# Optimization experiments

Hardware: AMD Instinct MI355X
Metric: run time of the kernel (lower is better)

## Reference

```python
import jax, jax.numpy as jnp
import numpy as np

N = 768          # number of atoms
DIM = 3
F = 128          # feature width
N_RBF = 32       # gaussian radial basis size
CUTOFF = 5.0
NUM_CHAINS = 4
T_IN_K = 300.0
TTIME = 20.0
KB = 8.617330337217213e-05   # Boltzmann constant, eV/K (ASE units.kB)
BOX = 24.8                   # box side so that ~26 neighbors/atom within cutoff
GAMMA = 1.0 / (CUTOFF / N_RBF) ** 2  # RBF width


def setup_inputs() -> dict:
    key = jax.random.key(0)
    ks = jax.random.split(key, 12)
    q = jax.random.uniform(ks[0], (N, DIM), dtype=jnp.float32) * BOX
    v = jax.random.normal(ks[1], (N, DIM), dtype=jnp.float32) * 0.01
    p_eta = jax.random.normal(ks[2], (NUM_CHAINS,), dtype=jnp.float32) * 0.1
    mass = jax.random.uniform(ks[3], (N,), dtype=jnp.float32, minval=1.0, maxval=20.0)
    atomic_numbers = jax.random.randint(ks[4], (N,), 0, 100, dtype=jnp.int32)
    embed = jax.random.normal(ks[5], (100, F), dtype=jnp.float32) * 0.1
    W1 = jax.random.normal(ks[6], (N_RBF, F), dtype=jnp.float32) / np.sqrt(N_RBF)
    b1 = jnp.zeros((F,), dtype=jnp.float32)
    W2 = jax.random.normal(ks[7], (F, F), dtype=jnp.float32) / np.sqrt(F)
    b2 = jnp.zeros((F,), dtype=jnp.float32)
    W3 = jax.random.normal(ks[8], (F, F), dtype=jnp.float32) / np.sqrt(F)
    w_out = jax.random.normal(ks[9], (F,), dtype=jnp.float32) / np.sqrt(F)
    return dict(v=v, q=q, p_eta=p_eta, mass=mass, embed=embed, W1=W1, b1=b1,
                W2=W2, b2=b2, W3=W3, w_out=w_out, atomic_numbers=atomic_numbers)


def _energy(q, atomic_numbers, embed, W1, b1, W2, b2, W3, w_out):
    """SchNet-style cutoff-graph potential energy (scalar)."""
    h = embed[atomic_numbers]                                   # [N,F]
    disp = q[:, None, :] - q[None, :, :]                        # [N,N,3]
    d2 = jnp.sum(disp * disp, axis=-1)                          # [N,N]
    eye = jnp.eye(N, dtype=bool)
    mask = (d2 < CUTOFF ** 2) & (~eye)                          # cutoff neighbor list (dense mask)
    d = jnp.sqrt(jnp.where(mask, d2, 1.0))                      # safe sqrt off-graph
    centers = jnp.linspace(0.0, CUTOFF, N_RBF, dtype=q.dtype)
    rbf = jnp.exp(-GAMMA * (d[..., None] - centers) ** 2)       # [N,N,n_rbf]
    filt = jax.nn.relu(rbf @ W1 + b1) @ W2 + b2                 # [N,N,F]
    filt = jnp.where(mask[..., None], filt, 0.0)
    m = jnp.einsum('ijf,jf->if', filt, h)                       # message aggregation
    h = h + jax.nn.relu(m @ W3)
    return jnp.sum(h @ w_out)


def reference(v, q, p_eta, mass, embed, W1, b1, W2, b2, W3, w_out, atomic_numbers):
    kT = T_IN_K * KB
    n_dof = N * DIM
    target_ke = 0.5 * n_dof * kT
    Q = 2.0 * jnp.array([n_dof * kT * TTIME ** 2] + [kT * TTIME ** 2] * (NUM_CHAINS - 1),
                        dtype=v.dtype)
    p = v * mass[:, None]                                       # momenta
    current_ke = 0.5 * jnp.sum(p * p / mass[:, None])
    # f = -dE/dq (torch: -results['energy_grad'])
    f = -jax.grad(_energy)(q, atomic_numbers, embed, W1, b1, W2, b2, W3, w_out)
    coupled_forces = (p_eta[0] * p.reshape(-1) / Q[0]).reshape(-1, 3)
    dvdt = (f - coupled_forces) / mass[:, None]
    dpeta_first = 2.0 * (current_ke - target_ke) - p_eta[0] * p_eta[1] / Q[1]
    dpeta_mid = p_eta[:-2] ** 2 / Q[:-2] - kT - p_eta[1:-1] * p_eta[2:] / Q[2:]
    dpeta_last = p_eta[-2] ** 2 / Q[-2] - kT
    dpeta_dt = jnp.concatenate([dpeta_first[None], dpeta_mid, dpeta_last[None]])
    return (dvdt, v, dpeta_dt)
```

## Files before the change

kernel.cpp:

```cpp
#include <hip/hip_runtime.h>
#include <math.h>

#define N_ATOMS 768
#define FD 128
#define NRBF 32
#define MAXN 64
#define PPF 32
#define NTHREADS 512
#define TST 136
#define RSTU 40

constexpr float  CUT2   = 25.0f;
constexpr float  GAMMA_ = 40.96f;
constexpr float  CSTEP  = 5.0f / 31.0f;
constexpr double KB_D   = 8.617330337217213e-05;
constexpr double KT_D   = 300.0 * KB_D;
constexpr float  KT_F   = (float)KT_D;
constexpr float  TARGET_KE = (float)(0.5 * 2304.0 * KT_D);
constexpr float  Q0_F   = (float)(2.0 * 2304.0 * KT_D * 400.0);
constexpr float  QI_F   = (float)(2.0 * KT_D * 400.0);

#define DVDT_OFF 0
#define V_OFF    (3 * N_ATOMS)
#define PETA_OFF (6 * N_ATOMS)

using short8v = __attribute__((ext_vector_type(8))) short;
using f32x4   = __attribute__((ext_vector_type(4))) float;

#define MFMA_B16 __builtin_amdgcn_mfma_f32_16x16x32_bf16

__device__ __forceinline__ unsigned short f2bf(float x) {
    unsigned int u = __float_as_uint(x);
    u += 0x7FFF + ((u >> 16) & 1);
    return (unsigned short)(u >> 16);
}
__device__ __forceinline__ float bf2f(unsigned short h) {
    return __uint_as_float(((unsigned int)h) << 16);
}


__global__ __launch_bounds__(256) void prep_kernel(
    const int* __restrict__ z, const float* __restrict__ embed,
    const float* __restrict__ W1, const float* __restrict__ W2,
    const float* __restrict__ W3,
    float* __restrict__ h, float* __restrict__ W3T,
    unsigned short* __restrict__ w1fh, unsigned short* __restrict__ w1fl,
    unsigned short* __restrict__ w2fh, unsigned short* __restrict__ w2fl,
    unsigned short* __restrict__ w2bh, unsigned short* __restrict__ w2bl,
    float* __restrict__ f_acc)
{
    int g = blockIdx.x * 256 + threadIdx.x;
    if (g < N_ATOMS * FD) h[g] = embed[z[g >> 7] * FD + (g & 127)];
    if (g < FD * FD) {
        int r = g >> 7, c = g & 127;
        float w = W2[g];
        unsigned short hb = f2bf(w);
        unsigned short lb = f2bf(w - bf2f(hb));
        w2bh[g] = hb;
        w2bl[g] = lb;
        w2fh[c * FD + r] = hb;
        w2fl[c * FD + r] = lb;
        W3T[c * FD + r] = W3[g];
        if (g < NRBF * FD) {
            float w1v = W1[g];
            unsigned short h1 = f2bf(w1v);
            w1fh[c * NRBF + r] = h1;
            w1fl[c * NRBF + r] = f2bf(w1v - bf2f(h1));
        }
    }
    if (g < 3 * N_ATOMS) f_acc[g] = 0.f;
}

__global__ __launch_bounds__(NTHREADS) void atom_kernel(
    const float* __restrict__ q,
    const unsigned short* __restrict__ w1fh, const unsigned short* __restrict__ w1fl,
    const float* __restrict__ b1,
    const unsigned short* __restrict__ w2fh, const unsigned short* __restrict__ w2fl,
    const unsigned short* __restrict__ w2bh, const unsigned short* __restrict__ w2bl,
    const float* __restrict__ b2, const float* __restrict__ h,
    const float* __restrict__ W3, const float* __restrict__ W3T,
    const float* __restrict__ wout,
    float* __restrict__ f_acc)
{
    __shared__ int   nj[MAXN];
    __shared__ float nd[MAXN], ndx[MAXN], ndy[MAXN], ndz[MAXN];
    __shared__ int   cnt_s;
    __shared__ __align__(16) unsigned short poolR[2 * PPF * RSTU];
    __shared__ __align__(16) unsigned short poolA[2 * PPF * TST];
    __shared__ float mrow[FD], gb[FD], mbrow[FD];
    __shared__ float sred[8 * PPF];

    unsigned short* rbf_h  = poolR;
    unsigned short* rbf_l  = poolR + PPF * RSTU;
    unsigned short* crbf_h = poolR;
    unsigned short* crbf_l = poolR + PPF * RSTU;
    unsigned short* a1h  = poolA;
    unsigned short* a1l  = poolA + PPF * TST;
    unsigned short* ts_h = poolA;
    unsigned short* ts_l = poolA + PPF * TST;

    int i = blockIdx.x, t = threadIdx.x;
    int wid = t >> 6, lane = t & 63;
    int lr = lane & 15, lg = lane >> 4;
    int c0 = wid * 16 + lr;

    if (t == 0) cnt_s = 0;
    __syncthreads();

    short8v w1h_r = *(const short8v*)(w1fh + c0 * NRBF + lg * 8);
    short8v w1l_r = *(const short8v*)(w1fl + c0 * NRBF + lg * 8);
    short8v w2f_h[4], w2f_l[4];
#pragma unroll
    for (int ks = 0; ks < 4; ks++) {
        int kb = ks * 32 + lg * 8;
        w2f_h[ks] = *(const short8v*)(w2fh + c0 * FD + kb);
        w2f_l[ks] = *(const short8v*)(w2fl + c0 * FD + kb);
    }
    float bb0  = b1[c0];
    float b2c0 = b2[c0];

    float qx = q[i*3], qy = q[i*3+1], qz = q[i*3+2];
    for (int j = t; j < N_ATOMS; j += NTHREADS) {
        if (j == i) continue;
        float dx = qx - q[j*3], dy = qy - q[j*3+1], dz = qz - q[j*3+2];
        float d2 = dx*dx + dy*dy + dz*dz;
        if (d2 < CUT2) {
            int p = atomicAdd(&cnt_s, 1);
            if (p < MAXN) { nj[p] = j; nd[p] = sqrtf(d2);
                            ndx[p] = dx; ndy[p] = dy; ndz[p] = dz; }
        }
    }
    __syncthreads();
    int cnt = min(cnt_s, MAXN);
    if (cnt == 0) return;

    float macc0 = 0.f;
    unsigned int mk0 = 0, mk1 = 0;

    float4 hj0[2];
#pragma unroll
    for (int e = 0; e < 2; e++) {
        int idx = t + e * NTHREADS;
        int p = idx >> 5, c4g = (idx & 31) * 4;
        hj0[e] = (p < cnt) ? *(const float4*)(h + nj[p] * FD + c4g)
                           : make_float4(0.f, 0.f, 0.f, 0.f);
    }

    auto fwd_pass = [&](int p0, unsigned int& mk_out) {
#pragma unroll
        for (int e = 0; e < 2; e++) {
            int idx = t + e * NTHREADS;
            int p = idx >> 5, k = idx & 31;
            int pp = p0 + p;
            float d = (pp < cnt) ? nd[pp] : 1.0f;
            float u = d - CSTEP * (float)k;
            float r = __expf(-GAMMA_ * u * u);
            unsigned short hb = f2bf(r);
            rbf_h[p * RSTU + k] = hb;
            rbf_l[p * RSTU + k] = f2bf(r - bf2f(hb));
        }
        __syncthreads();

        float h00[4], h10[4];
#pragma unroll
        for (int r = 0; r < 4; r++) {
            int pA = p0 + lg * 4 + r, pB = pA + 16;
            bool vA = pA < cnt, vB = pB < cnt;
            int jA = vA ? nj[pA] : 0, jB = vB ? nj[pB] : 0;
            h00[r] = vA ? h[jA * FD + c0] : 0.f;
            h10[r] = vB ? h[jB * FD + c0] : 0.f;
        }

        {
            f32x4 u00 = {bb0,bb0,bb0,bb0};
            f32x4 u10 = {bb0,bb0,bb0,bb0};
            short8v rh0 = *(const short8v*)(rbf_h + lr * RSTU + lg * 8);
            short8v rh1 = *(const short8v*)(rbf_h + (16+lr) * RSTU + lg * 8);
            short8v rl0 = *(const short8v*)(rbf_l + lr * RSTU + lg * 8);
            short8v rl1 = *(const short8v*)(rbf_l + (16+lr) * RSTU + lg * 8);
            u00 = MFMA_B16(rh0, w1h_r, u00, 0,0,0);
            u10 = MFMA_B16(rh1, w1h_r, u10, 0,0,0);
            u00 = MFMA_B16(rh0, w1l_r, u00, 0,0,0);
            u10 = MFMA_B16(rh1, w1l_r, u10, 0,0,0);
            u00 = MFMA_B16(rl0, w1h_r, u00, 0,0,0);
            u10 = MFMA_B16(rl1, w1h_r, u10, 0,0,0);
            unsigned int mk = 0;
#pragma unroll
            for (int r = 0; r < 4; r++) {
                int pA = lg * 4 + r, pB = 16 + lg * 4 + r;
                float v; unsigned short hb;
                if (u00[r] > 0.f) mk |= 1u << r;
                if (u10[r] > 0.f) mk |= 1u << (4 + r);
                v = fmaxf(u00[r], 0.f); hb = f2bf(v);
                a1h[pA * TST + c0] = hb; a1l[pA * TST + c0] = f2bf(v - bf2f(hb));
                v = fmaxf(u10[r], 0.f); hb = f2bf(v);
                a1h[pB * TST + c0] = hb; a1l[pB * TST + c0] = f2bf(v - bf2f(hb));
            }
            mk_out = mk;
        }
        __syncthreads();

        {
            f32x4 acc00 = {0.f,0.f,0.f,0.f};
            f32x4 acc10 = {0.f,0.f,0.f,0.f};
#pragma unroll
            for (int ks = 0; ks < 4; ks++) {
                int kb = ks * 32 + lg * 8;
                short8v ah0 = *(const short8v*)(a1h + (lr     ) * TST + kb);
                short8v ah1 = *(const short8v*)(a1h + (16 + lr) * TST + kb);
                short8v al0 = *(const short8v*)(a1l + (lr     ) * TST + kb);
                short8v al1 = *(const short8v*)(a1l + (16 + lr) * TST + kb);
                acc00 = MFMA_B16(ah0, w2f_h[ks], acc00, 0,0,0);
                acc10 = MFMA_B16(ah1, w2f_h[ks], acc10, 0,0,0);
                acc00 = MFMA_B16(ah0, w2f_l[ks], acc00, 0,0,0);
                acc10 = MFMA_B16(ah1, w2f_l[ks], acc10, 0,0,0);
                acc00 = MFMA_B16(al0, w2f_h[ks], acc00, 0,0,0);
                acc10 = MFMA_B16(al1, w2f_h[ks], acc10, 0,0,0);
            }
#pragma unroll
            for (int r = 0; r < 4; r++) {
                macc0 += (acc00[r] + b2c0) * h00[r] + (acc10[r] + b2c0) * h10[r];
            }
        }
    };

    fwd_pass(0, mk0);
    if (cnt > PPF) { __syncthreads(); fwd_pass(PPF, mk1); }

    short8v w2b_h[4], w2b_l[4];
#pragma unroll
    for (int ks = 0; ks < 4; ks++) {
        int kb = ks * 32 + lg * 8;
        w2b_h[ks] = *(const short8v*)(w2bh + c0 * FD + kb);
        w2b_l[ks] = *(const short8v*)(w2bl + c0 * FD + kb);
    }

    {
        float r0 = macc0 + __shfl_xor(macc0, 16, 64);
        r0 += __shfl_xor(r0, 32, 64);
        if (lg == 0) mrow[c0] = r0;
    }
    __syncthreads();

    {
        int f0h = lg * 32;
        float g = 0.f;
#pragma unroll
        for (int f4 = 0; f4 < 32; f4 += 4) {
            float4 w  = *(const float4*)(W3T + c0 * FD + f0h + f4);
            float4 mr = *(const float4*)(mrow + f0h + f4);
            g += mr.x*w.x + mr.y*w.y + mr.z*w.z + mr.w*w.w;
        }
        g += __shfl_xor(g, 16, 64);
        g += __shfl_xor(g, 32, 64);
        if (lg == 0) gb[c0] = (g > 0.f) ? wout[c0] : 0.f;
    }
    __syncthreads();
    {
        int f0h = lg * 32;
        float mb = 0.f;
#pragma unroll
        for (int f4 = 0; f4 < 32; f4 += 4) {
            float4 w  = *(const float4*)(W3 + c0 * FD + f0h + f4);
            float4 gv = *(const float4*)(gb + f0h + f4);
            mb += gv.x*w.x + gv.y*w.y + gv.z*w.z + gv.w*w.w;
        }
        mb += __shfl_xor(mb, 16, 64);
        mb += __shfl_xor(mb, 32, 64);
        if (lg == 0) mbrow[c0] = mb;
    }
    __syncthreads();

    float iax = 0.f, iay = 0.f, iaz = 0.f;

    auto bwd_pass = [&](int p0, unsigned int mk, bool first) {
#pragma unroll
        for (int e = 0; e < 2; e++) {
            int idx = t + e * NTHREADS;
            int p = idx >> 5, k = idx & 31;
            int pp = p0 + p;
            float d = (pp < cnt) ? nd[pp] : 1.0f;
            float u = d - CSTEP * (float)k;
            float r = __expf(-GAMMA_ * u * u);
            float cd = -2.f * GAMMA_ * u * r;
            unsigned short hc = f2bf(cd);
            crbf_h[p * RSTU + k] = hc;
            crbf_l[p * RSTU + k] = f2bf(cd - bf2f(hc));
        }
#pragma unroll
        for (int e = 0; e < 2; e++) {
            int idx = t + e * NTHREADS;
            int p = idx >> 5, c4g = (idx & 31) * 4;
            int pp = p0 + p;
            ushort4 hv = {0,0,0,0}, lv = {0,0,0,0};
            if (pp < cnt) {
                float4 mb4 = *(const float4*)(mbrow + c4g);
                float4 hj4 = first ? hj0[e]
                                   : *(const float4*)(h + nj[pp] * FD + c4g);
                float v0 = mb4.x*hj4.x, v1 = mb4.y*hj4.y;
                float v2 = mb4.z*hj4.z, v3 = mb4.w*hj4.w;
                hv.x = f2bf(v0); lv.x = f2bf(v0 - bf2f(hv.x));
                hv.y = f2bf(v1); lv.y = f2bf(v1 - bf2f(hv.y));
                hv.z = f2bf(v2); lv.z = f2bf(v2 - bf2f(hv.z));
                hv.w = f2bf(v3); lv.w = f2bf(v3 - bf2f(hv.w));
            }
            *(ushort4*)(ts_h + p * TST + c4g) = hv;
            *(ushort4*)(ts_l + p * TST + c4g) = lv;
        }
        __syncthreads();

        f32x4 e00 = {0.f,0.f,0.f,0.f};
        f32x4 e10 = {0.f,0.f,0.f,0.f};
        {
            short8v ch0 = *(const short8v*)(crbf_h + lr * RSTU + lg * 8);
            short8v ch1 = *(const short8v*)(crbf_h + (16+lr) * RSTU + lg * 8);
            short8v cl0 = *(const short8v*)(crbf_l + lr * RSTU + lg * 8);
            short8v cl1 = *(const short8v*)(crbf_l + (16+lr) * RSTU + lg * 8);
            e00 = MFMA_B16(ch0, w1h_r, e00, 0,0,0);
            e10 = MFMA_B16(ch1, w1h_r, e10, 0,0,0);
            e00 = MFMA_B16(ch0, w1l_r, e00, 0,0,0);
            e10 = MFMA_B16(ch1, w1l_r, e10, 0,0,0);
            e00 = MFMA_B16(cl0, w1h_r, e00, 0,0,0);
            e10 = MFMA_B16(cl1, w1h_r, e10, 0,0,0);
        }
#pragma unroll
        for (int r = 0; r < 4; r++) {
            e00[r] = (mk & (1u <<  r      )) ? e00[r] : 0.f;
            e10[r] = (mk & (1u << (4 + r))) ? e10[r] : 0.f;
        }

        f32x4 acc00 = {0.f,0.f,0.f,0.f};
        f32x4 acc10 = {0.f,0.f,0.f,0.f};
#pragma unroll
        for (int ks = 0; ks < 4; ks++) {
            int kb = ks * 32 + lg * 8;
            short8v ah0 = *(const short8v*)(ts_h + (lr     ) * TST + kb);
            short8v ah1 = *(const short8v*)(ts_h + (16 + lr) * TST + kb);
            short8v al0 = *(const short8v*)(ts_l + (lr     ) * TST + kb);
            short8v al1 = *(const short8v*)(ts_l + (16 + lr) * TST + kb);
            acc00 = MFMA_B16(ah0, w2b_h[ks], acc00, 0,0,0);
            acc10 = MFMA_B16(ah1, w2b_h[ks], acc10, 0,0,0);
            acc00 = MFMA_B16(ah0, w2b_l[ks], acc00, 0,0,0);
            acc10 = MFMA_B16(ah1, w2b_l[ks], acc10, 0,0,0);
            acc00 = MFMA_B16(al0, w2b_h[ks], acc00, 0,0,0);
            acc10 = MFMA_B16(al1, w2b_h[ks], acc10, 0,0,0);
        }

        float part8[8];
#pragma unroll
        for (int r = 0; r < 4; r++) {
            part8[r]     = acc00[r] * e00[r];
            part8[4 + r] = acc10[r] * e10[r];
        }
#pragma unroll
        for (int mask = 1; mask < 16; mask <<= 1) {
#pragma unroll
            for (int e = 0; e < 8; e++) part8[e] += __shfl_xor(part8[e], mask, 64);
        }
        if (lr == 0) {
#pragma unroll
            for (int r = 0; r < 4; r++) {
                sred[wid * PPF + lg * 4 + r]      = part8[r];
                sred[wid * PPF + 16 + lg * 4 + r] = part8[4 + r];
            }
        }
        __syncthreads();

        if (t < PPF && p0 + t < cnt) {
            float s = 0.f;
#pragma unroll
            for (int w = 0; w < 8; w++) s += sred[w * PPF + t];
            int pp = p0 + t;
            float coef = s / nd[pp];
            float fx = coef * ndx[pp];
            float fy = coef * ndy[pp];
            float fz = coef * ndz[pp];
            iax += fx; iay += fy; iaz += fz;
            atomicAdd(f_acc + nj[pp]*3 + 0, fx);
            atomicAdd(f_acc + nj[pp]*3 + 1, fy);
            atomicAdd(f_acc + nj[pp]*3 + 2, fz);
        }
    };

    bwd_pass(0, mk0, true);
    if (cnt > PPF) { __syncthreads(); bwd_pass(PPF, mk1, false); }

    if (t < PPF) {
#pragma unroll
        for (int mask = 1; mask < 32; mask <<= 1) {
            iax += __shfl_xor(iax, mask, 64);
            iay += __shfl_xor(iay, mask, 64);
            iaz += __shfl_xor(iaz, mask, 64);
        }
        if (t == 0) {
            atomicAdd(f_acc + i*3 + 0, -iax);
            atomicAdd(f_acc + i*3 + 1, -iay);
            atomicAdd(f_acc + i*3 + 2, -iaz);
        }
    }
}

__global__ __launch_bounds__(256) void fin_kernel(
    const float* __restrict__ v, const float* __restrict__ mass,
    const float* __restrict__ p_eta, const float* __restrict__ f_acc,
    float* __restrict__ out)
{
    __shared__ float red[256];
    int t = threadIdx.x;
    float ke = 0.f;
    float c = p_eta[0] / Q0_F;
    for (int idx = t; idx < 3 * N_ATOMS; idx += 256) {
        int a = idx / 3;
        float vv = v[idx], mi = mass[a];
        out[DVDT_OFF + idx] = (f_acc[idx] - c * vv * mi) / mi;
        out[V_OFF + idx] = vv;
        ke += 0.5f * mi * vv * vv;
    }
    red[t] = ke;
    __syncthreads();
    for (int s = 128; s > 0; s >>= 1) {
        if (t < s) red[t] += red[t + s];
        __syncthreads();
    }
    if (t == 0) {
        float k0 = red[0];
        float e0 = p_eta[0], e1 = p_eta[1], e2 = p_eta[2], e3 = p_eta[3];
        out[PETA_OFF + 0] = 2.f * (k0 - TARGET_KE) - e0 * e1 / QI_F;
        out[PETA_OFF + 1] = e0 * e0 / Q0_F - KT_F - e1 * e2 / QI_F;
        out[PETA_OFF + 2] = e1 * e1 / QI_F - KT_F - e2 * e3 / QI_F;
        out[PETA_OFF + 3] = e2 * e2 / QI_F - KT_F;
    }
}

extern "C" void kernel_launch(void* const* d_in, const int* in_sizes, int n_in,
                              void* d_out, int out_size, void* d_ws, size_t ws_size,
                              hipStream_t stream)
{
    const float* v     = (const float*)d_in[0];
    const float* q     = (const float*)d_in[1];
    const float* p_eta = (const float*)d_in[2];
    const float* mass  = (const float*)d_in[3];
    const float* embed = (const float*)d_in[4];
    const float* W1    = (const float*)d_in[5];
    const float* b1    = (const float*)d_in[6];
    const float* W2    = (const float*)d_in[7];
    const float* b2    = (const float*)d_in[8];
    const float* W3    = (const float*)d_in[9];
    const float* wout  = (const float*)d_in[10];
    const int*   z     = (const int*)d_in[11];
    float* out = (float*)d_out;

    float* h     = (float*)d_ws;
    float* W3T   = h + N_ATOMS * FD;
    float* f_acc = W3T + FD * FD;
    unsigned short* w2bh = (unsigned short*)(f_acc + 3 * N_ATOMS);
    unsigned short* w2bl = w2bh + FD * FD;
    unsigned short* w2fh = w2bl + FD * FD;
    unsigned short* w2fl = w2fh + FD * FD;
    unsigned short* w1fh = w2fl + FD * FD;
    unsigned short* w1fl = w1fh + NRBF * FD;

    prep_kernel<<<384, 256, 0, stream>>>(z, embed, W1, W2, W3, h, W3T,
                                         w1fh, w1fl, w2fh, w2fl, w2bh, w2bl,
                                         f_acc);
    atom_kernel<<<N_ATOMS, NTHREADS, 0, stream>>>(q, w1fh, w1fl, b1, w2fh, w2fl,
                                                  w2bh, w2bl, b2, h, W3, W3T, wout,
                                                  f_acc);
    fin_kernel<<<1, 256, 0, stream>>>(v, mass, p_eta, f_acc, out);
}
```

Baseline: 127.8 us.

## Merge two 32-neighbor passes into one 64-neighbor pass per atom block

Result: no change. 127.0 us (-0.6%).

```diff
diff --git a/kernel.cpp b/kernel.cpp
--- a/kernel.cpp
+++ b/kernel.cpp
@@ -5,7 +5,6 @@
 #define FD 128
 #define NRBF 32
 #define MAXN 64
-#define PPF 32
 #define NTHREADS 512
 #define TST 136
 #define RSTU 40
@@ -85,19 +84,19 @@
     __shared__ int   nj[MAXN];
     __shared__ float nd[MAXN], ndx[MAXN], ndy[MAXN], ndz[MAXN];
     __shared__ int   cnt_s;
-    __shared__ __align__(16) unsigned short poolR[2 * PPF * RSTU];
-    __shared__ __align__(16) unsigned short poolA[2 * PPF * TST];
+    __shared__ __align__(16) unsigned short poolR[2 * MAXN * RSTU];
+    __shared__ __align__(16) unsigned short poolA[2 * MAXN * TST];
     __shared__ float mrow[FD], gb[FD], mbrow[FD];
-    __shared__ float sred[8 * PPF];
+    __shared__ float sred[8 * MAXN];
 
     unsigned short* rbf_h  = poolR;
-    unsigned short* rbf_l  = poolR + PPF * RSTU;
+    unsigned short* rbf_l  = poolR + MAXN * RSTU;
     unsigned short* crbf_h = poolR;
-    unsigned short* crbf_l = poolR + PPF * RSTU;
+    unsigned short* crbf_l = poolR + MAXN * RSTU;
     unsigned short* a1h  = poolA;
-    unsigned short* a1l  = poolA + PPF * TST;
+    unsigned short* a1l  = poolA + MAXN * TST;
     unsigned short* ts_h = poolA;
-    unsigned short* ts_l = poolA + PPF * TST;
+    unsigned short* ts_l = poolA + MAXN * TST;
 
     int i = blockIdx.x, t = threadIdx.x;
     int wid = t >> 6, lane = t & 63;
@@ -133,9 +132,10 @@
     __syncthreads();
     int cnt = min(cnt_s, MAXN);
     if (cnt == 0) return;
+    bool heavy = cnt > 32;
 
     float macc0 = 0.f;
-    unsigned int mk0 = 0, mk1 = 0;
+    unsigned int mk = 0;
 
     float4 hj0[2];
 #pragma unroll
@@ -146,86 +146,136 @@
                            : make_float4(0.f, 0.f, 0.f, 0.f);
     }
 
-    auto fwd_pass = [&](int p0, unsigned int& mk_out) {
-#pragma unroll
-        for (int e = 0; e < 2; e++) {
+    {
+        int nit = heavy ? 4 : 2;
+        for (int e = 0; e < nit; e++) {
             int idx = t + e * NTHREADS;
             int p = idx >> 5, k = idx & 31;
-            int pp = p0 + p;
-            float d = (pp < cnt) ? nd[pp] : 1.0f;
+            float d = (p < cnt) ? nd[p] : 1.0f;
             float u = d - CSTEP * (float)k;
             float r = __expf(-GAMMA_ * u * u);
             unsigned short hb = f2bf(r);
             rbf_h[p * RSTU + k] = hb;
             rbf_l[p * RSTU + k] = f2bf(r - bf2f(hb));
         }
-        __syncthreads();
-
-        float h00[4], h10[4];
+    }
+    __syncthreads();
+
+    float h00[4], h10[4], h20[4], h30[4];
+#pragma unroll
+    for (int r = 0; r < 4; r++) {
+        int pA = lg * 4 + r, pB = pA + 16;
+        bool vA = pA < cnt, vB = pB < cnt;
+        h00[r] = vA ? h[nj[pA] * FD + c0] : 0.f;
+        h10[r] = vB ? h[nj[pB] * FD + c0] : 0.f;
+        h20[r] = 0.f; h30[r] = 0.f;
+    }
+    if (heavy) {
 #pragma unroll
         for (int r = 0; r < 4; r++) {
-            int pA = p0 + lg * 4 + r, pB = pA + 16;
-            bool vA = pA < cnt, vB = pB < cnt;
-            int jA = vA ? nj[pA] : 0, jB = vB ? nj[pB] : 0;
-            h00[r] = vA ? h[jA * FD + c0] : 0.f;
-            h10[r] = vB ? h[jB * FD + c0] : 0.f;
-        }
-
-        {
-            f32x4 u00 = {bb0,bb0,bb0,bb0};
-            f32x4 u10 = {bb0,bb0,bb0,bb0};
-            short8v rh0 = *(const short8v*)(rbf_h + lr * RSTU + lg * 8);
-            short8v rh1 = *(const short8v*)(rbf_h + (16+lr) * RSTU + lg * 8);
-            short8v rl0 = *(const short8v*)(rbf_l + lr * RSTU + lg * 8);
-            short8v rl1 = *(const short8v*)(rbf_l + (16+lr) * RSTU + lg * 8);
-            u00 = MFMA_B16(rh0, w1h_r, u00, 0,0,0);
-            u10 = MFMA_B16(rh1, w1h_r, u10, 0,0,0);
-            u00 = MFMA_B16(rh0, w1l_r, u00, 0,0,0);
-            u10 = MFMA_B16(rh1, w1l_r, u10, 0,0,0);
-            u00 = MFMA_B16(rl0, w1h_r, u00, 0,0,0);
-            u10 = MFMA_B16(rl1, w1h_r, u10, 0,0,0);
-            unsigned int mk = 0;
+            int pC = 32 + lg * 4 + r, pD = pC + 16;
+            bool vC = pC < cnt, vD = pD < cnt;
+            h20[r] = vC ? h[nj[pC] * FD + c0] : 0.f;
+            h30[r] = vD ? h[nj[pD] * FD + c0] : 0.f;
+        }
+    }
+
+    {
+        f32x4 u00 = {bb0,bb0,bb0,bb0};
+        f32x4 u10 = {bb0,bb0,bb0,bb0};
+        short8v rh0 = *(const short8v*)(rbf_h + lr * RSTU + lg * 8);
+        short8v rh1 = *(const short8v*)(rbf_h + (16+lr) * RSTU + lg * 8);
+        short8v rl0 = *(const short8v*)(rbf_l + lr * RSTU + lg * 8);
+        short8v rl1 = *(const short8v*)(rbf_l + (16+lr) * RSTU + lg * 8);
+        u00 = MFMA_B16(rh0, w1h_r, u00, 0,0,0);
+        u10 = MFMA_B16(rh1, w1h_r, u10, 0,0,0);
+        u00 = MFMA_B16(rh0, w1l_r, u00, 0,0,0);
+        u10 = MFMA_B16(rh1, w1l_r, u10, 0,0,0);
+        u00 = MFMA_B16(rl0, w1h_r, u00, 0,0,0);
+        u10 = MFMA_B16(rl1, w1h_r, u10, 0,0,0);
+#pragma unroll
+        for (int r = 0; r < 4; r++) {
+            int pA = lg * 4 + r, pB = 16 + lg * 4 + r;
+            float v; unsigned short hb;
+            if (u00[r] > 0.f) mk |= 1u << r;
+            if (u10[r] > 0.f) mk |= 1u << (4 + r);
+            v = fmaxf(u00[r], 0.f); hb = f2bf(v);
+            a1h[pA * TST + c0] = hb; a1l[pA * TST + c0] = f2bf(v - bf2f(hb));
+            v = fmaxf(u10[r], 0.f); hb = f2bf(v);
+            a1h[pB * TST + c0] = hb; a1l[pB * TST + c0] = f2bf(v - bf2f(hb));
+        }
+        if (heavy) {
+            f32x4 u20 = {bb0,bb0,bb0,bb0};
+            f32x4 u30 = {bb0,bb0,bb0,bb0};
+            short8v rh2 = *(const short8v*)(rbf_h + (32+lr) * RSTU + lg * 8);
+            short8v rh3 = *(const short8v*)(rbf_h + (48+lr) * RSTU + lg * 8);
+            short8v rl2 = *(const short8v*)(rbf_l + (32+lr) * RSTU + lg * 8);
+            short8v rl3 = *(const short8v*)(rbf_l + (48+lr) * RSTU + lg * 8);
+            u20 = MFMA_B16(rh2, w1h_r, u20, 0,0,0);
+            u30 = MFMA_B16(rh3, w1h_r, u30, 0,0,0);
+            u20 = MFMA_B16(rh2, w1l_r, u20, 0,0,0);
+            u30 = MFMA_B16(rh3, w1l_r, u30, 0,0,0);
+            u20 = MFMA_B16(rl2, w1h_r, u20, 0,0,0);
+            u30 = MFMA_B16(rl3, w1h_r, u30, 0,0,0);
 #pragma unroll
             for (int r = 0; r < 4; r++) {
-                int pA = lg * 4 + r, pB = 16 + lg * 4 + r;
+                int pC = 32 + lg * 4 + r, pD = 48 + lg * 4 + r;
                 float v; unsigned short hb;
-                if (u00[r] > 0.f) mk |= 1u << r;
-                if (u10[r] > 0.f) mk |= 1u << (4 + r);
-                v = fmaxf(u00[r], 0.f); hb = f2bf(v);
-                a1h[pA * TST + c0] = hb; a1l[pA * TST + c0] = f2bf(v - bf2f(hb));
-                v = fmaxf(u10[r], 0.f); hb = f2bf(v);
-                a1h[pB * TST + c0] = hb; a1l[pB * TST + c0] = f2bf(v - bf2f(hb));
-            }
-            mk_out = mk;
-        }
-        __syncthreads();
-
-        {
-            f32x4 acc00 = {0.f,0.f,0.f,0.f};
-            f32x4 acc10 = {0.f,0.f,0.f,0.f};
+                if (u20[r] > 0.f) mk |= 1u << (8 + r);
+                if (u30[r] > 0.f) mk |= 1u << (12 + r);
+                v = fmaxf(u20[r], 0.f); hb = f2bf(v);
+                a1h[pC * TST + c0] = hb; a1l[pC * TST + c0] = f2bf(v - bf2f(hb));
+                v = fmaxf(u30[r], 0.f); hb = f2bf(v);
+                a1h[pD * TST + c0] = hb; a1l[pD * TST + c0] = f2bf(v - bf2f(hb));
+            }
+        }
+    }
+    __syncthreads();
+
+    {
+        f32x4 acc00 = {0.f,0.f,0.f,0.f};
+        f32x4 acc10 = {0.f,0.f,0.f,0.f};
+#pragma unroll
+        for (int ks = 0; ks < 4; ks++) {
+            int kb = ks * 32 + lg * 8;
+            short8v ah0 = *(const short8v*)(a1h + (lr     ) * TST + kb);
+            short8v ah1 = *(const short8v*)(a1h + (16 + lr) * TST + kb);
+            short8v al0 = *(const short8v*)(a1l + (lr     ) * TST + kb);
+            short8v al1 = *(const short8v*)(a1l + (16 + lr) * TST + kb);
+            acc00 = MFMA_B16(ah0, w2f_h[ks], acc00, 0,0,0);
+            acc10 = MFMA_B16(ah1, w2f_h[ks], acc10, 0,0,0);
+            acc00 = MFMA_B16(ah0, w2f_l[ks], acc00, 0,0,0);
+            acc10 = MFMA_B16(ah1, w2f_l[ks], acc10, 0,0,0);
+            acc00 = MFMA_B16(al0, w2f_h[ks], acc00, 0,0,0);
+            acc10 = MFMA_B16(al1, w2f_h[ks], acc10, 0,0,0);
+        }
+#pragma unroll
+        for (int r = 0; r < 4; r++) {
+            macc0 += (acc00[r] + b2c0) * h00[r] + (acc10[r] + b2c0) * h10[r];
+        }
+        if (heavy) {
+            f32x4 acc20 = {0.f,0.f,0.f,0.f};
+            f32x4 acc30 = {0.f,0.f,0.f,0.f};
 #pragma unroll
             for (int ks = 0; ks < 4; ks++) {
                 int kb = ks * 32 + lg * 8;
-                short8v ah0 = *(const short8v*)(a1h + (lr     ) * TST + kb);
-                short8v ah1 = *(const short8v*)(a1h + (16 + lr) * TST + kb);
-                short8v al0 = *(const short8v*)(a1l + (lr     ) * TST + kb);
-                short8v al1 = *(const short8v*)(a1l + (16 + lr) * TST + kb);
-                acc00 = MFMA_B16(ah0, w2f_h[ks], acc00, 0,0,0);
-                acc10 = MFMA_B16(ah1, w2f_h[ks], acc10, 0,0,0);
-                acc00 = MFMA_B16(ah0, w2f_l[ks], acc00, 0,0,0);
-                acc10 = MFMA_B16(ah1, w2f_l[ks], acc10, 0,0,0);
-                acc00 = MFMA_B16(al0, w2f_h[ks], acc00, 0,0,0);
-                acc10 = MFMA_B16(al1, w2f_h[ks], acc10, 0,0,0);
+                short8v ah2 = *(const short8v*)(a1h + (32 + lr) * TST + kb);
+                short8v ah3 = *(const short8v*)(a1h + (48 + lr) * TST + kb);
+                short8v al2 = *(const short8v*)(a1l + (32 + lr) * TST + kb);
+                short8v al3 = *(const short8v*)(a1l + (48 + lr) * TST + kb);
+                acc20 = MFMA_B16(ah2, w2f_h[ks], acc20, 0,0,0);
+                acc30 = MFMA_B16(ah3, w2f_h[ks], acc30, 0,0,0);
+                acc20 = MFMA_B16(ah2, w2f_l[ks], acc20, 0,0,0);
+                acc30 = MFMA_B16(ah3, w2f_l[ks], acc30, 0,0,0);
+                acc20 = MFMA_B16(al2, w2f_h[ks], acc20, 0,0,0);
+                acc30 = MFMA_B16(al3, w2f_h[ks], acc30, 0,0,0);
             }
 #pragma unroll
             for (int r = 0; r < 4; r++) {
-                macc0 += (acc00[r] + b2c0) * h00[r] + (acc10[r] + b2c0) * h10[r];
-            }
-        }
-    };
-
-    fwd_pass(0, mk0);
-    if (cnt > PPF) { __syncthreads(); fwd_pass(PPF, mk1); }
+                macc0 += (acc20[r] + b2c0) * h20[r] + (acc30[r] + b2c0) * h30[r];
+            }
+        }
+    }
 
     short8v w2b_h[4], w2b_l[4];
 #pragma unroll
@@ -271,15 +321,12 @@
     }
     __syncthreads();
 
-    float iax = 0.f, iay = 0.f, iaz = 0.f;
-
-    auto bwd_pass = [&](int p0, unsigned int mk, bool first) {
-#pragma unroll
-        for (int e = 0; e < 2; e++) {
+    {
+        int nit = heavy ? 4 : 2;
+        for (int e = 0; e < nit; e++) {
             int idx = t + e * NTHREADS;
             int p = idx >> 5, k = idx & 31;
-            int pp = p0 + p;
-            float d = (pp < cnt) ? nd[pp] : 1.0f;
+            float d = (p < cnt) ? nd[p] : 1.0f;
             float u = d - CSTEP * (float)k;
             float r = __expf(-GAMMA_ * u * u);
             float cd = -2.f * GAMMA_ * u * r;
@@ -287,16 +334,14 @@
             crbf_h[p * RSTU + k] = hc;
             crbf_l[p * RSTU + k] = f2bf(cd - bf2f(hc));
         }
-#pragma unroll
-        for (int e = 0; e < 2; e++) {
+        for (int e = 0; e < nit; e++) {
             int idx = t + e * NTHREADS;
             int p = idx >> 5, c4g = (idx & 31) * 4;
-            int pp = p0 + p;
             ushort4 hv = {0,0,0,0}, lv = {0,0,0,0};
-            if (pp < cnt) {
+            if (p < cnt) {
                 float4 mb4 = *(const float4*)(mbrow + c4g);
-                float4 hj4 = first ? hj0[e]
-                                   : *(const float4*)(h + nj[pp] * FD + c4g);
+                float4 hj4 = (e < 2) ? hj0[e]
+                                     : *(const float4*)(h + nj[p] * FD + c4g);
                 float v0 = mb4.x*hj4.x, v1 = mb4.y*hj4.y;
                 float v2 = mb4.z*hj4.z, v3 = mb4.w*hj4.w;
                 hv.x = f2bf(v0); lv.x = f2bf(v0 - bf2f(hv.x));
@@ -307,8 +352,10 @@
             *(ushort4*)(ts_h + p * TST + c4g) = hv;
             *(ushort4*)(ts_l + p * TST + c4g) = lv;
         }
-        __syncthreads();
-
+    }
+    __syncthreads();
+
+    {
         f32x4 e00 = {0.f,0.f,0.f,0.f};
         f32x4 e10 = {0.f,0.f,0.f,0.f};
         {
@@ -360,34 +407,87 @@
         if (lr == 0) {
 #pragma unroll
             for (int r = 0; r < 4; r++) {
-                sred[wid * PPF + lg * 4 + r]      = part8[r];
-                sred[wid * PPF + 16 + lg * 4 + r] = part8[4 + r];
-            }
-        }
-        __syncthreads();
-
-        if (t < PPF && p0 + t < cnt) {
-            float s = 0.f;
-#pragma unroll
-            for (int w = 0; w < 8; w++) s += sred[w * PPF + t];
-            int pp = p0 + t;
-            float coef = s / nd[pp];
-            float fx = coef * ndx[pp];
-            float fy = coef * ndy[pp];
-            float fz = coef * ndz[pp];
-            iax += fx; iay += fy; iaz += fz;
-            atomicAdd(f_acc + nj[pp]*3 + 0, fx);
-            atomicAdd(f_acc + nj[pp]*3 + 1, fy);
-            atomicAdd(f_acc + nj[pp]*3 + 2, fz);
-        }
-    };
-
-    bwd_pass(0, mk0, true);
-    if (cnt > PPF) { __syncthreads(); bwd_pass(PPF, mk1, false); }
-
-    if (t < PPF) {
-#pragma unroll
-        for (int mask = 1; mask < 32; mask <<= 1) {
+                sred[wid * MAXN + lg * 4 + r]      = part8[r];
+                sred[wid * MAXN + 16 + lg * 4 + r] = part8[4 + r];
+            }
+        }
+
+        if (heavy) {
+            f32x4 e20 = {0.f,0.f,0.f,0.f};
+            f32x4 e30 = {0.f,0.f,0.f,0.f};
+            {
+                short8v ch2 = *(const short8v*)(crbf_h + (32+lr) * RSTU + lg * 8);
+                short8v ch3 = *(const short8v*)(crbf_h + (48+lr) * RSTU + lg * 8);
+                short8v cl2 = *(const short8v*)(crbf_l + (32+lr) * RSTU + lg * 8);
+                short8v cl3 = *(const short8v*)(crbf_l + (48+lr) * RSTU + lg * 8);
+                e20 = MFMA_B16(ch2, w1h_r, e20, 0,0,0);
+                e30 = MFMA_B16(ch3, w1h_r, e30, 0,0,0);
+                e20 = MFMA_B16(ch2, w1l_r, e20, 0,0,0);
+                e30 = MFMA_B16(ch3, w1l_r, e30, 0,0,0);
+                e20 = MFMA_B16(cl2, w1h_r, e20, 0,0,0);
+                e30 = MFMA_B16(cl3, w1h_r, e30, 0,0,0);
+            }
+#pragma unroll
+            for (int r = 0; r < 4; r++) {
+                e20[r] = (mk & (1u << (8 + r)))  ? e20[r] : 0.f;
+                e30[r] = (mk & (1u << (12 + r))) ? e30[r] : 0.f;
+            }
+            f32x4 acc20 = {0.f,0.f,0.f,0.f};
+            f32x4 acc30 = {0.f,0.f,0.f,0.f};
+#pragma unroll
+            for (int ks = 0; ks < 4; ks++) {
+                int kb = ks * 32 + lg * 8;
+                short8v ah2 = *(const short8v*)(ts_h + (32 + lr) * TST + kb);
+                short8v ah3 = *(const short8v*)(ts_h + (48 + lr) * TST + kb);
+                short8v al2 = *(const short8v*)(ts_l + (32 + lr) * TST + kb);
+                short8v al3 = *(const short8v*)(ts_l + (48 + lr) * TST + kb);
+                acc20 = MFMA_B16(ah2, w2b_h[ks], acc20, 0,0,0);
+                acc30 = MFMA_B16(ah3, w2b_h[ks], acc30, 0,0,0);
+                acc20 = MFMA_B16(ah2, w2b_l[ks], acc20, 0,0,0);
+                acc30 = MFMA_B16(ah3, w2b_l[ks], acc30, 0,0,0);
+                acc20 = MFMA_B16(al2, w2b_h[ks], acc20, 0,0,0);
+                acc30 = MFMA_B16(al3, w2b_h[ks], acc30, 0,0,0);
+            }
+            float p8[8];
+#pragma unroll
+            for (int r = 0; r < 4; r++) {
+                p8[r]     = acc20[r] * e20[r];
+                p8[4 + r] = acc30[r] * e30[r];
+            }
+#pragma unroll
+            for (int mask = 1; mask < 16; mask <<= 1) {
+#pragma unroll
+                for (int e = 0; e < 8; e++) p8[e] += __shfl_xor(p8[e], mask, 64);
+            }
+            if (lr == 0) {
+#pragma unroll
+                for (int r = 0; r < 4; r++) {
+                    sred[wid * MAXN + 32 + lg * 4 + r] = p8[r];
+                    sred[wid * MAXN + 48 + lg * 4 + r] = p8[4 + r];
+                }
+            }
+        }
+    }
+    __syncthreads();
+
+    float iax = 0.f, iay = 0.f, iaz = 0.f;
+    if (t < MAXN && t < cnt) {
+        float s = 0.f;
+#pragma unroll
+        for (int w = 0; w < 8; w++) s += sred[w * MAXN + t];
+        float coef = s / nd[t];
+        float fx = coef * ndx[t];
+        float fy = coef * ndy[t];
+        float fz = coef * ndz[t];
+        iax = fx; iay = fy; iaz = fz;
+        atomicAdd(f_acc + nj[t]*3 + 0, fx);
+        atomicAdd(f_acc + nj[t]*3 + 1, fy);
+        atomicAdd(f_acc + nj[t]*3 + 2, fz);
+    }
+
+    if (t < MAXN) {
+#pragma unroll
+        for (int mask = 1; mask < 64; mask <<= 1) {
             iax += __shfl_xor(iax, mask, 64);
             iay += __shfl_xor(iay, mask, 64);
             iaz += __shfl_xor(iaz, mask, 64);
```

## Process all neighbors in one pass using 16-row MFMA tiles

Applied to the files above, without the earlier changes.

After: 122.9 us. 1.04x faster.

```diff
diff --git a/kernel.cpp b/kernel.cpp
--- a/kernel.cpp
+++ b/kernel.cpp
@@ -5,7 +5,6 @@
 #define FD 128
 #define NRBF 32
 #define MAXN 64
-#define PPF 32
 #define NTHREADS 512
 #define TST 136
 #define RSTU 40
@@ -85,19 +84,19 @@
     __shared__ int   nj[MAXN];
     __shared__ float nd[MAXN], ndx[MAXN], ndy[MAXN], ndz[MAXN];
     __shared__ int   cnt_s;
-    __shared__ __align__(16) unsigned short poolR[2 * PPF * RSTU];
-    __shared__ __align__(16) unsigned short poolA[2 * PPF * TST];
+    __shared__ __align__(16) unsigned short poolR[2 * MAXN * RSTU];
+    __shared__ __align__(16) unsigned short poolA[2 * MAXN * TST];
     __shared__ float mrow[FD], gb[FD], mbrow[FD];
-    __shared__ float sred[8 * PPF];
+    __shared__ float sred[8 * MAXN];
 
     unsigned short* rbf_h  = poolR;
-    unsigned short* rbf_l  = poolR + PPF * RSTU;
+    unsigned short* rbf_l  = poolR + MAXN * RSTU;
     unsigned short* crbf_h = poolR;
-    unsigned short* crbf_l = poolR + PPF * RSTU;
+    unsigned short* crbf_l = poolR + MAXN * RSTU;
     unsigned short* a1h  = poolA;
-    unsigned short* a1l  = poolA + PPF * TST;
+    unsigned short* a1l  = poolA + MAXN * TST;
     unsigned short* ts_h = poolA;
-    unsigned short* ts_l = poolA + PPF * TST;
+    unsigned short* ts_l = poolA + MAXN * TST;
 
     int i = blockIdx.x, t = threadIdx.x;
     int wid = t >> 6, lane = t & 63;
@@ -133,9 +132,10 @@
     __syncthreads();
     int cnt = min(cnt_s, MAXN);
     if (cnt == 0) return;
+    int ntl = (cnt + 15) >> 4;
 
     float macc0 = 0.f;
-    unsigned int mk0 = 0, mk1 = 0;
+    unsigned int mk = 0;
 
     float4 hj0[2];
 #pragma unroll
@@ -146,86 +146,59 @@
                            : make_float4(0.f, 0.f, 0.f, 0.f);
     }
 
-    auto fwd_pass = [&](int p0, unsigned int& mk_out) {
-#pragma unroll
-        for (int e = 0; e < 2; e++) {
-            int idx = t + e * NTHREADS;
-            int p = idx >> 5, k = idx & 31;
-            int pp = p0 + p;
-            float d = (pp < cnt) ? nd[pp] : 1.0f;
-            float u = d - CSTEP * (float)k;
-            float r = __expf(-GAMMA_ * u * u);
-            unsigned short hb = f2bf(r);
-            rbf_h[p * RSTU + k] = hb;
-            rbf_l[p * RSTU + k] = f2bf(r - bf2f(hb));
-        }
-        __syncthreads();
-
-        float h00[4], h10[4];
+    for (int e = 0; e < ntl; e++) {
+        int idx = t + e * NTHREADS;
+        int p = idx >> 5, k = idx & 31;
+        float d = (p < cnt) ? nd[p] : 1.0f;
+        float u = d - CSTEP * (float)k;
+        float r = __expf(-GAMMA_ * u * u);
+        unsigned short hb = f2bf(r);
+        rbf_h[p * RSTU + k] = hb;
+        rbf_l[p * RSTU + k] = f2bf(r - bf2f(hb));
+    }
+    __syncthreads();
+
+    for (int tl = 0; tl < ntl; tl++) {
+        int rb = tl * 16;
+        f32x4 u0 = {bb0, bb0, bb0, bb0};
+        short8v rh = *(const short8v*)(rbf_h + (rb + lr) * RSTU + lg * 8);
+        short8v rl = *(const short8v*)(rbf_l + (rb + lr) * RSTU + lg * 8);
+        u0 = MFMA_B16(rh, w1h_r, u0, 0,0,0);
+        u0 = MFMA_B16(rh, w1l_r, u0, 0,0,0);
+        u0 = MFMA_B16(rl, w1h_r, u0, 0,0,0);
 #pragma unroll
         for (int r = 0; r < 4; r++) {
-            int pA = p0 + lg * 4 + r, pB = pA + 16;
-            bool vA = pA < cnt, vB = pB < cnt;
-            int jA = vA ? nj[pA] : 0, jB = vB ? nj[pB] : 0;
-            h00[r] = vA ? h[jA * FD + c0] : 0.f;
-            h10[r] = vB ? h[jB * FD + c0] : 0.f;
-        }
-
-        {
-            f32x4 u00 = {bb0,bb0,bb0,bb0};
-            f32x4 u10 = {bb0,bb0,bb0,bb0};
-            short8v rh0 = *(const short8v*)(rbf_h + lr * RSTU + lg * 8);
-            short8v rh1 = *(const short8v*)(rbf_h + (16+lr) * RSTU + lg * 8);
-            short8v rl0 = *(const short8v*)(rbf_l + lr * RSTU + lg * 8);
-            short8v rl1 = *(const short8v*)(rbf_l + (16+lr) * RSTU + lg * 8);
-            u00 = MFMA_B16(rh0, w1h_r, u00, 0,0,0);
-            u10 = MFMA_B16(rh1, w1h_r, u10, 0,0,0);
-            u00 = MFMA_B16(rh0, w1l_r, u00, 0,0,0);
-            u10 = MFMA_B16(rh1, w1l_r, u10, 0,0,0);
-            u00 = MFMA_B16(rl0, w1h_r, u00, 0,0,0);
-            u10 = MFMA_B16(rl1, w1h_r, u10, 0,0,0);
-            unsigned int mk = 0;
-#pragma unroll
-            for (int r = 0; r < 4; r++) {
-                int pA = lg * 4 + r, pB = 16 + lg * 4 + r;
-                float v; unsigned short hb;
-                if (u00[r] > 0.f) mk |= 1u << r;
-                if (u10[r] > 0.f) mk |= 1u << (4 + r);
-                v = fmaxf(u00[r], 0.f); hb = f2bf(v);
-                a1h[pA * TST + c0] = hb; a1l[pA * TST + c0] = f2bf(v - bf2f(hb));
-                v = fmaxf(u10[r], 0.f); hb = f2bf(v);
-                a1h[pB * TST + c0] = hb; a1l[pB * TST + c0] = f2bf(v - bf2f(hb));
-            }
-            mk_out = mk;
-        }
-        __syncthreads();
-
-        {
-            f32x4 acc00 = {0.f,0.f,0.f,0.f};
-            f32x4 acc10 = {0.f,0.f,0.f,0.f};
-#pragma unroll
-            for (int ks = 0; ks < 4; ks++) {
-                int kb = ks * 32 + lg * 8;
-                short8v ah0 = *(const short8v*)(a1h + (lr     ) * TST + kb);
-                short8v ah1 = *(const short8v*)(a1h + (16 + lr) * TST + kb);
-                short8v al0 = *(const short8v*)(a1l + (lr     ) * TST + kb);
-                short8v al1 = *(const short8v*)(a1l + (16 + lr) * TST + kb);
-                acc00 = MFMA_B16(ah0, w2f_h[ks], acc00, 0,0,0);
-                acc10 = MFMA_B16(ah1, w2f_h[ks], acc10, 0,0,0);
-                acc00 = MFMA_B16(ah0, w2f_l[ks], acc00, 0,0,0);
-                acc10 = MFMA_B16(ah1, w2f_l[ks], acc10, 0,0,0);
-                acc00 = MFMA_B16(al0, w2f_h[ks], acc00, 0,0,0);
-                acc10 = MFMA_B16(al1, w2f_h[ks], acc10, 0,0,0);
-            }
-#pragma unroll
-            for (int r = 0; r < 4; r++) {
-                macc0 += (acc00[r] + b2c0) * h00[r] + (acc10[r] + b2c0) * h10[r];
-            }
-        }
-    };
-
-    fwd_pass(0, mk0);
-    if (cnt > PPF) { __syncthreads(); fwd_pass(PPF, mk1); }
+            int p = rb + lg * 4 + r;
+            if (u0[r] > 0.f) mk |= 1u << (4 * tl + r);
+            float v = fmaxf(u0[r], 0.f);
+            unsigned short hb = f2bf(v);
+            a1h[p * TST + c0] = hb;
+            a1l[p * TST + c0] = f2bf(v - bf2f(hb));
+        }
+    }
+    __syncthreads();
+
+    for (int tl = 0; tl < ntl; tl++) {
+        int rb = tl * 16;
+        float hv[4];
+#pragma unroll
+        for (int r = 0; r < 4; r++) {
+            int p = rb + lg * 4 + r;
+            hv[r] = (p < cnt) ? h[nj[p] * FD + c0] : 0.f;
+        }
+        f32x4 acc = {0.f, 0.f, 0.f, 0.f};
+#pragma unroll
+        for (int ks = 0; ks < 4; ks++) {
+            int kb = ks * 32 + lg * 8;
+            short8v ah = *(const short8v*)(a1h + (rb + lr) * TST + kb);
+            short8v al = *(const short8v*)(a1l + (rb + lr) * TST + kb);
+            acc = MFMA_B16(ah, w2f_h[ks], acc, 0,0,0);
+            acc = MFMA_B16(ah, w2f_l[ks], acc, 0,0,0);
+            acc = MFMA_B16(al, w2f_h[ks], acc, 0,0,0);
+        }
+#pragma unroll
+        for (int r = 0; r < 4; r++) macc0 += (acc[r] + b2c0) * hv[r];
+    }
 
     short8v w2b_h[4], w2b_l[4];
 #pragma unroll
@@ -271,123 +244,97 @@
     }
     __syncthreads();
 
-    float iax = 0.f, iay = 0.f, iaz = 0.f;
-
-    auto bwd_pass = [&](int p0, unsigned int mk, bool first) {
-#pragma unroll
-        for (int e = 0; e < 2; e++) {
-            int idx = t + e * NTHREADS;
-            int p = idx >> 5, k = idx & 31;
-            int pp = p0 + p;
-            float d = (pp < cnt) ? nd[pp] : 1.0f;
-            float u = d - CSTEP * (float)k;
-            float r = __expf(-GAMMA_ * u * u);
-            float cd = -2.f * GAMMA_ * u * r;
-            unsigned short hc = f2bf(cd);
-            crbf_h[p * RSTU + k] = hc;
-            crbf_l[p * RSTU + k] = f2bf(cd - bf2f(hc));
-        }
-#pragma unroll
-        for (int e = 0; e < 2; e++) {
-            int idx = t + e * NTHREADS;
-            int p = idx >> 5, c4g = (idx & 31) * 4;
-            int pp = p0 + p;
-            ushort4 hv = {0,0,0,0}, lv = {0,0,0,0};
-            if (pp < cnt) {
-                float4 mb4 = *(const float4*)(mbrow + c4g);
-                float4 hj4 = first ? hj0[e]
-                                   : *(const float4*)(h + nj[pp] * FD + c4g);
-                float v0 = mb4.x*hj4.x, v1 = mb4.y*hj4.y;
-                float v2 = mb4.z*hj4.z, v3 = mb4.w*hj4.w;
-                hv.x = f2bf(v0); lv.x = f2bf(v0 - bf2f(hv.x));
-                hv.y = f2bf(v1); lv.y = f2bf(v1 - bf2f(hv.y));
-                hv.z = f2bf(v2); lv.z = f2bf(v2 - bf2f(hv.z));
-                hv.w = f2bf(v3); lv.w = f2bf(v3 - bf2f(hv.w));
-            }
-            *(ushort4*)(ts_h + p * TST + c4g) = hv;
-            *(ushort4*)(ts_l + p * TST + c4g) = lv;
-        }
-        __syncthreads();
-
-        f32x4 e00 = {0.f,0.f,0.f,0.f};
-        f32x4 e10 = {0.f,0.f,0.f,0.f};
+    for (int e = 0; e < ntl; e++) {
+        int idx = t + e * NTHREADS;
+        int p = idx >> 5, k = idx & 31;
+        float d = (p < cnt) ? nd[p] : 1.0f;
+        float u = d - CSTEP * (float)k;
+        float r = __expf(-GAMMA_ * u * u);
+        float cd = -2.f * GAMMA_ * u * r;
+        unsigned short hc = f2bf(cd);
+        crbf_h[p * RSTU + k] = hc;
+        crbf_l[p * RSTU + k] = f2bf(cd - bf2f(hc));
+    }
+    for (int e = 0; e < ntl; e++) {
+        int idx = t + e * NTHREADS;
+        int p = idx >> 5, c4g = (idx & 31) * 4;
+        ushort4 hv = {0,0,0,0}, lv = {0,0,0,0};
+        if (p < cnt) {
+            float4 mb4 = *(const float4*)(mbrow + c4g);
+            float4 hj4 = (e < 2) ? hj0[e]
+                                 : *(const float4*)(h + nj[p] * FD + c4g);
+            float v0 = mb4.x*hj4.x, v1 = mb4.y*hj4.y;
+            float v2 = mb4.z*hj4.z, v3 = mb4.w*hj4.w;
+            hv.x = f2bf(v0); lv.x = f2bf(v0 - bf2f(hv.x));
+            hv.y = f2bf(v1); lv.y = f2bf(v1 - bf2f(hv.y));
+            hv.z = f2bf(v2); lv.z = f2bf(v2 - bf2f(hv.z));
+            hv.w = f2bf(v3); lv.w = f2bf(v3 - bf2f(hv.w));
+        }
+        *(ushort4*)(ts_h + p * TST + c4g) = hv;
+        *(ushort4*)(ts_l + p * TST + c4g) = lv;
+    }
+    __syncthreads();
+
+    for (int tl = 0; tl < ntl; tl++) {
+        int rb = tl * 16;
+        f32x4 ef = {0.f, 0.f, 0.f, 0.f};
         {
-            short8v ch0 = *(const short8v*)(crbf_h + lr * RSTU + lg * 8);
-            short8v ch1 = *(const short8v*)(crbf_h + (16+lr) * RSTU + lg * 8);
-            short8v cl0 = *(const short8v*)(crbf_l + lr * RSTU + lg * 8);
-            short8v cl1 = *(const short8v*)(crbf_l + (16+lr) * RSTU + lg * 8);
-            e00 = MFMA_B16(ch0, w1h_r, e00, 0,0,0);
-            e10 = MFMA_B16(ch1, w1h_r, e10, 0,0,0);
-            e00 = MFMA_B16(ch0, w1l_r, e00, 0,0,0);
-            e10 = MFMA_B16(ch1, w1l_r, e10, 0,0,0);
-            e00 = MFMA_B16(cl0, w1h_r, e00, 0,0,0);
-            e10 = MFMA_B16(cl1, w1h_r, e10, 0,0,0);
-        }
-#pragma unroll
-        for (int r = 0; r < 4; r++) {
-            e00[r] = (mk & (1u <<  r      )) ? e00[r] : 0.f;
-            e10[r] = (mk & (1u << (4 + r))) ? e10[r] : 0.f;
-        }
-
-        f32x4 acc00 = {0.f,0.f,0.f,0.f};
-        f32x4 acc10 = {0.f,0.f,0.f,0.f};
+            short8v ch = *(const short8v*)(crbf_h + (rb + lr) * RSTU + lg * 8);
+            short8v cl = *(const short8v*)(crbf_l + (rb + lr) * RSTU + lg * 8);
+            ef = MFMA_B16(ch, w1h_r, ef, 0,0,0);
+            ef = MFMA_B16(ch, w1l_r, ef, 0,0,0);
+            ef = MFMA_B16(cl, w1h_r, ef, 0,0,0);
+        }
+        unsigned int mt = (mk >> (4 * tl)) & 0xFu;
+#pragma unroll
+        for (int r = 0; r < 4; r++)
+            ef[r] = (mt & (1u << r)) ? ef[r] : 0.f;
+
+        f32x4 acc = {0.f, 0.f, 0.f, 0.f};
 #pragma unroll
         for (int ks = 0; ks < 4; ks++) {
             int kb = ks * 32 + lg * 8;
-            short8v ah0 = *(const short8v*)(ts_h + (lr     ) * TST + kb);
-            short8v ah1 = *(const short8v*)(ts_h + (16 + lr) * TST + kb);
-            short8v al0 = *(const short8v*)(ts_l + (lr     ) * TST + kb);
-            short8v al1 = *(const short8v*)(ts_l + (16 + lr) * TST + kb);
-            acc00 = MFMA_B16(ah0, w2b_h[ks], acc00, 0,0,0);
-            acc10 = MFMA_B16(ah1, w2b_h[ks], acc10, 0,0,0);
-            acc00 = MFMA_B16(ah0, w2b_l[ks], acc00, 0,0,0);
-            acc10 = MFMA_B16(ah1, w2b_l[ks], acc10, 0,0,0);
-            acc00 = MFMA_B16(al0, w2b_h[ks], acc00, 0,0,0);
-            acc10 = MFMA_B16(al1, w2b_h[ks], acc10, 0,0,0);
-        }
-
-        float part8[8];
-#pragma unroll
-        for (int r = 0; r < 4; r++) {
-            part8[r]     = acc00[r] * e00[r];
-            part8[4 + r] = acc10[r] * e10[r];
-        }
+            short8v ah = *(const short8v*)(ts_h + (rb + lr) * TST + kb);
+            short8v al = *(const short8v*)(ts_l + (rb + lr) * TST + kb);
+            acc = MFMA_B16(ah, w2b_h[ks], acc, 0,0,0);
+            acc = MFMA_B16(ah, w2b_l[ks], acc, 0,0,0);
+            acc = MFMA_B16(al, w2b_h[ks], acc, 0,0,0);
+        }
+
+        float p4[4];
+#pragma unroll
+        for (int r = 0; r < 4; r++) p4[r] = acc[r] * ef[r];
 #pragma unroll
         for (int mask = 1; mask < 16; mask <<= 1) {
 #pragma unroll
-            for (int e = 0; e < 8; e++) part8[e] += __shfl_xor(part8[e], mask, 64);
+            for (int e = 0; e < 4; e++) p4[e] += __shfl_xor(p4[e], mask, 64);
         }
         if (lr == 0) {
 #pragma unroll
-            for (int r = 0; r < 4; r++) {
-                sred[wid * PPF + lg * 4 + r]      = part8[r];
-                sred[wid * PPF + 16 + lg * 4 + r] = part8[4 + r];
-            }
-        }
-        __syncthreads();
-
-        if (t < PPF && p0 + t < cnt) {
-            float s = 0.f;
-#pragma unroll
-            for (int w = 0; w < 8; w++) s += sred[w * PPF + t];
-            int pp = p0 + t;
-            float coef = s / nd[pp];
-            float fx = coef * ndx[pp];
-            float fy = coef * ndy[pp];
-            float fz = coef * ndz[pp];
-            iax += fx; iay += fy; iaz += fz;
-            atomicAdd(f_acc + nj[pp]*3 + 0, fx);
-            atomicAdd(f_acc + nj[pp]*3 + 1, fy);
-            atomicAdd(f_acc + nj[pp]*3 + 2, fz);
-        }
-    };
-
-    bwd_pass(0, mk0, true);
-    if (cnt > PPF) { __syncthreads(); bwd_pass(PPF, mk1, false); }
-
-    if (t < PPF) {
-#pragma unroll
-        for (int mask = 1; mask < 32; mask <<= 1) {
+            for (int r = 0; r < 4; r++)
+                sred[wid * MAXN + rb + lg * 4 + r] = p4[r];
+        }
+    }
+    __syncthreads();
+
+    float iax = 0.f, iay = 0.f, iaz = 0.f;
+    if (t < MAXN && t < cnt) {
+        float s = 0.f;
+#pragma unroll
+        for (int w = 0; w < 8; w++) s += sred[w * MAXN + t];
+        float coef = s / nd[t];
+        float fx = coef * ndx[t];
+        float fy = coef * ndy[t];
+        float fz = coef * ndz[t];
+        iax = fx; iay = fy; iaz = fz;
+        atomicAdd(f_acc + nj[t]*3 + 0, fx);
+        atomicAdd(f_acc + nj[t]*3 + 1, fy);
+        atomicAdd(f_acc + nj[t]*3 + 2, fz);
+    }
+
+    if (t < MAXN) {
+#pragma unroll
+        for (int mask = 1; mask < 64; mask <<= 1) {
             iax += __shfl_xor(iax, mask, 64);
             iay += __shfl_xor(iay, mask, 64);
             iaz += __shfl_xor(iaz, mask, 64);
```
